# Kernel optimization log

Hardware: AMD Instinct MI355X
Metric: run time of the kernel (lower is better)

Reference implementation:

```python
import jax, jax.numpy as jnp
import numpy as np

N = 50000      # nodes
E = 1600000    # edges (before self loops)
B = 512        # graphs
D = 128        # gcn dim (constant across the 3 GAT layers)
H = 1024       # hidden_dim
O = 128        # output_dim
NEG_SLOPE = 0.2


def setup_inputs() -> dict:
    key = jax.random.key(0)
    ks = jax.random.split(key, 24)
    inp = {
        "x": jax.random.normal(ks[0], (N, D), jnp.float32),
        "edge_index": jax.random.randint(ks[1], (2, E), 0, N, dtype=jnp.int64),
        "edge_weight": jax.random.uniform(ks[2], (E,), jnp.float32),
        "batch": jnp.sort(jax.random.randint(ks[3], (N,), 0, B, dtype=jnp.int64)),
    }
    s = 1.0 / np.sqrt(D)
    for i in range(3):
        k = 4 + 4 * i
        inp[f"W{i+1}"] = jax.random.normal(ks[k], (D, D), jnp.float32) * s
        inp[f"as{i+1}"] = jax.random.normal(ks[k + 1], (D,), jnp.float32) * s
        inp[f"ad{i+1}"] = jax.random.normal(ks[k + 2], (D,), jnp.float32) * s
        inp[f"b{i+1}"] = jnp.zeros((D,), jnp.float32)
    inp["Wf1"] = jax.random.normal(ks[16], (D, H), jnp.float32) * s
    inp["bf1"] = jnp.zeros((H,), jnp.float32)
    inp["Wf2"] = jax.random.normal(ks[17], (H, O), jnp.float32) * (1.0 / np.sqrt(H))
    inp["bf2"] = jnp.zeros((O,), jnp.float32)
    return inp


def gat_conv(x, src, dst, W, a_src, a_dst, b):
    """PyG GATConv, heads=1: gather -> leakyrelu -> segment softmax -> scatter-add."""
    h = x @ W                                   # [N, D]
    e = jax.nn.leaky_relu(jnp.take(h @ a_src, src) + jnp.take(h @ a_dst, dst), NEG_SLOPE)  # [E']
    m = jax.ops.segment_max(e, dst, num_segments=N)
    ex = jnp.exp(e - m[dst])
    denom = jax.ops.segment_sum(ex, dst, num_segments=N)
    alpha = ex / denom[dst]                      # segment softmax over incoming edges
    out = jax.ops.segment_sum(alpha[:, None] * h[src], dst, num_segments=N)
    return out + b


def reference(x, edge_index, edge_weight, batch,
              W1, as1, ad1, b1, W2, as2, ad2, b2, W3, as3, ad3, b3,
              Wf1, bf1, Wf2, bf2):
    # GATConv adds self loops; edge_weight is unused by GATConv (faithful to original)
    loop = jnp.arange(N, dtype=edge_index.dtype)
    src = jnp.concatenate([edge_index[0], loop])
    dst = jnp.concatenate([edge_index[1], loop])

    h = gat_conv(x, src, dst, W1, as1, ad1, b1)
    h = jax.nn.relu(gat_conv(h, src, dst, W2, as2, ad2, b2))
    h = jax.nn.relu(gat_conv(h, src, dst, W3, as3, ad3, b3))

    # global mean pool (gep)
    sums = jax.ops.segment_sum(h, batch, num_segments=B)        # [B, D]
    counts = jax.ops.segment_sum(jnp.ones((N,), h.dtype), batch, num_segments=B)
    pooled = sums / jnp.maximum(counts, 1.0)[:, None]

    # MLP head; dropout is identity at inference
    o = jax.nn.relu(pooled) @ Wf1 + bf1
    o = jax.nn.relu(o) @ Wf2 + bf2
    return o
```

## Files before the change

kernel.cpp:

```cpp
#include <hip/hip_runtime.h>
#include <cstdint>
#include <cstddef>

#define NEG_SLOPE 0.2f

typedef _Float16 f16x8 __attribute__((ext_vector_type(8)));
typedef float f32x4v __attribute__((ext_vector_type(4)));

__device__ __forceinline__ unsigned enc_f(float f) {
  unsigned u = __float_as_uint(f);
  return (u & 0x80000000u) ? ~u : (u | 0x80000000u);
}
__device__ __forceinline__ float dec_f(unsigned u) {
  return (u & 0x80000000u) ? __uint_as_float(u ^ 0x80000000u) : __uint_as_float(~u);
}

#define AST 136
#define WST 136
#define HST 132
#define SMEM_BYTES (64 * AST * 2 + 128 * WST * 2)

__global__ void k_bounds(const int* __restrict__ batch, int N, int B,
                         int* __restrict__ gstart, unsigned* __restrict__ maxPart,
                         int* __restrict__ counts) {
  int n = blockIdx.x * blockDim.x + threadIdx.x;
  if (n < 768) maxPart[n] = 0u;
  if (n >= N) return;
  counts[n] = 0;
  int cur = batch[n];
  if (n == 0) {
    for (int g = 0; g <= cur; g++) gstart[g] = 0;
  } else {
    int prev = batch[n - 1];
    for (int g = prev + 1; g <= cur; g++) gstart[g] = n;
  }
  if (n == N - 1) {
    for (int g = cur + 1; g <= B; g++) gstart[g] = N;
  }
}

__global__ void k_count_rank(const int* __restrict__ dst, int E,
                             int* counts, int* __restrict__ rank) {
  int e = blockIdx.x * blockDim.x + threadIdx.x;
  if (e < E) rank[e] = atomicAdd(&counts[dst[e]], 1);
}

__global__ __launch_bounds__(1024) void k_scan1(const int* __restrict__ counts, int N,
                                                int* __restrict__ row_ptr, int* __restrict__ part) {
  __shared__ int tmp[1024];
  int t = threadIdx.x;
  int i = blockIdx.x * 1024 + t;
  int v = (i < N) ? 1 + counts[i] : 0;
  tmp[t] = v;
  __syncthreads();
  for (int off = 1; off < 1024; off <<= 1) {
    int u = (t >= off) ? tmp[t - off] : 0;
    __syncthreads();
    tmp[t] += u;
    __syncthreads();
  }
  if (i < N) row_ptr[i + 1] = tmp[t];
  if (t == 1023) part[blockIdx.x] = tmp[t];
}

__global__ __launch_bounds__(1024) void k_scan3(int* __restrict__ row_ptr,
                                                const int* __restrict__ part, int N) {
  __shared__ int s_off;
  int bi = blockIdx.x;
  if (threadIdx.x == 0) {
    int run = 0;
    for (int b = 0; b < bi; b++) run += part[b];
    s_off = run;
    if (bi == 0) row_ptr[0] = 0;
  }
  __syncthreads();
  int i = bi * 1024 + threadIdx.x;
  if (i < N) row_ptr[i + 1] += s_off;
}

__device__ __forceinline__ void gemm_body(char* smem, float* redmax, int bx,
                                          const float* __restrict__ A32,
                                          const unsigned short* __restrict__ A16,
                                          const float* __restrict__ W,
                                          unsigned short* __restrict__ hb,
                                          const float* __restrict__ asrc,
                                          const float* __restrict__ adst,
                                          float* __restrict__ sv, float* __restrict__ dv,
                                          unsigned* __restrict__ maxSlot, int M) {
  _Float16* Ah = (_Float16*)smem;
  _Float16* Wt = (_Float16*)(smem + 64 * AST * 2);
  float*    hS = (float*)(smem + 64 * AST * 2);
  int t = threadIdx.x;
  int rowbase = bx * 64;

  if (A16) {
    for (int i = t; i < 64 * 16; i += 256) {
      int r = i >> 4, c8 = (i & 15) << 3;
      int gr = rowbase + r;
      uint4 v = make_uint4(0u, 0u, 0u, 0u);
      if (gr < M) v = *(const uint4*)&A16[(size_t)gr * 128 + c8];
      *(uint4*)&Ah[r * AST + c8] = v;
    }
  } else {
    for (int i = t; i < 64 * 32; i += 256) {
      int r = i >> 5, c4 = (i & 31) << 2;
      int gr = rowbase + r;
      float4 v = make_float4(0.f, 0.f, 0.f, 0.f);
      if (gr < M) v = *(const float4*)&A32[(size_t)gr * 128 + c4];
      _Float16 tmp[4] = {(_Float16)v.x, (_Float16)v.y, (_Float16)v.z, (_Float16)v.w};
      *(short4*)&Ah[r * AST + c4] = *(short4*)tmp;
    }
  }
  for (int i = t; i < 128 * 32; i += 256) {
    int r = i >> 5, c4 = (i & 31) << 2;
    float4 v = *(const float4*)&W[(size_t)r * 128 + c4];
    Wt[(c4 + 0) * WST + r] = (_Float16)v.x;
    Wt[(c4 + 1) * WST + r] = (_Float16)v.y;
    Wt[(c4 + 2) * WST + r] = (_Float16)v.z;
    Wt[(c4 + 3) * WST + r] = (_Float16)v.w;
  }
  __syncthreads();

  int wave = t >> 6, lane = t & 63, quad = lane >> 4, l15 = lane & 15;
  f32x4v acc[4][2];
#pragma unroll
  for (int mt = 0; mt < 4; mt++)
#pragma unroll
    for (int nt = 0; nt < 2; nt++) {
      acc[mt][nt][0] = 0.f; acc[mt][nt][1] = 0.f; acc[mt][nt][2] = 0.f; acc[mt][nt][3] = 0.f;
    }

#pragma unroll
  for (int s = 0; s < 4; s++) {
    int k0 = (s << 5) + (quad << 3);
    f16x8 af[4], bf[2];
#pragma unroll
    for (int mt = 0; mt < 4; mt++)
      af[mt] = *(f16x8*)&Ah[(mt * 16 + l15) * AST + k0];
#pragma unroll
    for (int nt = 0; nt < 2; nt++)
      bf[nt] = *(f16x8*)&Wt[(wave * 32 + nt * 16 + l15) * WST + k0];
#pragma unroll
    for (int mt = 0; mt < 4; mt++)
#pragma unroll
      for (int nt = 0; nt < 2; nt++)
        acc[mt][nt] = __builtin_amdgcn_mfma_f32_16x16x32_f16(af[mt], bf[nt], acc[mt][nt], 0, 0, 0);
  }
  __syncthreads();

#pragma unroll
  for (int mt = 0; mt < 4; mt++)
#pragma unroll
    for (int nt = 0; nt < 2; nt++)
#pragma unroll
      for (int rr = 0; rr < 4; rr++)
        hS[(mt * 16 + quad * 4 + rr) * HST + wave * 32 + nt * 16 + l15] = acc[mt][nt][rr];
  __syncthreads();

  int tx = t & 31, ty = t >> 5;
  float4 av  = *(const float4*)&asrc[tx * 4];
  float4 adv = *(const float4*)&adst[tx * 4];
  float wmax = -1e30f;
#pragma unroll
  for (int r8 = 0; r8 < 8; r8++) {
    int row = r8 * 8 + ty;
    int gr = rowbase + row;
    float4 hv = *(float4*)&hS[row * HST + tx * 4];
    float ps = hv.x * av.x + hv.y * av.y + hv.z * av.z + hv.w * av.w;
    float pd = hv.x * adv.x + hv.y * adv.y + hv.z * adv.z + hv.w * adv.w;
#pragma unroll
    for (int mask = 16; mask; mask >>= 1) {
      ps += __shfl_xor(ps, mask);
      pd += __shfl_xor(pd, mask);
    }
    if (gr < M) {
      _Float16 hq[4] = {(_Float16)hv.x, (_Float16)hv.y, (_Float16)hv.z, (_Float16)hv.w};
      *(uint2*)&hb[(size_t)gr * 128 + tx * 4] = *(uint2*)hq;
      if (tx == 0) { sv[gr] = ps; dv[gr] = pd; wmax = fmaxf(wmax, ps); }
    }
  }
#pragma unroll
  for (int mask = 32; mask; mask >>= 1) wmax = fmaxf(wmax, __shfl_xor(wmax, mask));
  if ((t & 63) == 0) redmax[t >> 6] = wmax;
  __syncthreads();
  if (t == 0) {
    float mx = fmaxf(fmaxf(redmax[0], redmax[1]), fmaxf(redmax[2], redmax[3]));
    atomicMax(&maxSlot[bx & 255], enc_f(mx));
  }
}

__global__ __launch_bounds__(256) void k_fill_gemm(const int* __restrict__ src,
                                                   const int* __restrict__ dst,
                                                   const int* __restrict__ rank, int E, int N,
                                                   const int* __restrict__ row_ptr,
                                                   int* __restrict__ col,
                                                   const float* __restrict__ A32,
                                                   const float* __restrict__ W,
                                                   unsigned short* __restrict__ hb,
                                                   const float* __restrict__ asrc,
                                                   const float* __restrict__ adst,
                                                   float* __restrict__ sv, float* __restrict__ dv,
                                                   unsigned* __restrict__ maxSlot, int Gg) {
  __shared__ __align__(16) char smem[SMEM_BYTES];
  __shared__ float redmax[4];
  int b = (int)blockIdx.x;
  bool isGemm = ((b % 9) == 4) && ((b / 9) < Gg);
  if (isGemm) {
    gemm_body(smem, redmax, b / 9, A32, (const unsigned short*)nullptr, W,
              hb, asrc, adst, sv, dv, maxSlot, N);
  } else {
    int nGemmBefore = (b >= 4) ? min((b - 4) / 9 + 1, Gg) : 0;
    int i = (b - nGemmBefore) * 256 + threadIdx.x;
    if (i < N) col[row_ptr[i]] = i;
    int e = i - N;
    if (e >= 0 && e < E) col[row_ptr[dst[e]] + 1 + rank[e]] = src[e];
  }
}

__global__ __launch_bounds__(256) void k_gemm_fused(const unsigned short* __restrict__ A16,
                                                    const float* __restrict__ W,
                                                    unsigned short* __restrict__ hb,
                                                    const float* __restrict__ asrc,
                                                    const float* __restrict__ adst,
                                                    float* __restrict__ sv, float* __restrict__ dv,
                                                    unsigned* __restrict__ maxSlot, int M) {
  __shared__ __align__(16) char smem[SMEM_BYTES];
  __shared__ float redmax[4];
  gemm_body(smem, redmax, (int)blockIdx.x, (const float*)nullptr, A16, W,
            hb, asrc, adst, sv, dv, maxSlot, M);
}

__global__ __launch_bounds__(256) void k_agg(const unsigned short* __restrict__ hb,
                                             const float* __restrict__ sv,
                                             const float* __restrict__ dv,
                                             const int* __restrict__ row_ptr,
                                             const int* __restrict__ col,
                                             const float* __restrict__ bias,
                                             const unsigned* __restrict__ maxSlot,
                                             unsigned short* __restrict__ out16,
                                             int N, int relu) {
  int wid = (int)((blockIdx.x * (size_t)blockDim.x + threadIdx.x) >> 6);
  int lane = threadIdx.x & 63;
  if (wid >= N) return;

  unsigned mp = max(max(maxSlot[lane], maxSlot[lane + 64]),
                    max(maxSlot[lane + 128], maxSlot[lane + 192]));
#pragma unroll
  for (int off = 32; off; off >>= 1) mp = max(mp, __shfl_xor(mp, off));
  float maxS = dec_f(mp);

  int beg = row_ptr[wid], end = row_ptr[wid + 1];
  float dn = dv[wid];
  float m = maxS + dn;
  m = (m > 0.f) ? m : NEG_SLOPE * m;

  int g = lane >> 4, sub = lane & 15;
  const uint32_t* hbu = (const uint32_t*)hb;
  float acc[8];
#pragma unroll
  for (int k = 0; k < 8; k++) acc[k] = 0.f;
  float dsum = 0.f;

  int j = beg + g;
  float w0 = 0.f, w1 = 0.f, w2 = 0.f;
  uint4 h0 = make_uint4(0u, 0u, 0u, 0u);
  uint4 h1 = make_uint4(0u, 0u, 0u, 0u);
  uint4 h2 = make_uint4(0u, 0u, 0u, 0u);
  if (j < end) {
    int sn = col[j];
    float e = sv[sn] + dn;
    e = (e > 0.f) ? e : NEG_SLOPE * e;
    w0 = __expf(e - m);
    h0 = *(const uint4*)(hbu + (size_t)sn * 64 + sub * 4);
  }
  if (j + 4 < end) {
    int sn = col[j + 4];
    float e = sv[sn] + dn;
    e = (e > 0.f) ? e : NEG_SLOPE * e;
    w1 = __expf(e - m);
    h1 = *(const uint4*)(hbu + (size_t)sn * 64 + sub * 4);
  }
  if (j + 8 < end) {
    int sn = col[j + 8];
    float e = sv[sn] + dn;
    e = (e > 0.f) ? e : NEG_SLOPE * e;
    w2 = __expf(e - m);
    h2 = *(const uint4*)(hbu + (size_t)sn * 64 + sub * 4);
  }
  j += 12;
  while (j < end) {
    dsum += w0;
    {
      const _Float16* hp = (const _Float16*)&h0;
#pragma unroll
      for (int k = 0; k < 8; k++) acc[k] += w0 * (float)hp[k];
    }
    w0 = w1; h0 = h1;
    w1 = w2; h1 = h2;
    int sn = col[j];
    float e = sv[sn] + dn;
    e = (e > 0.f) ? e : NEG_SLOPE * e;
    w2 = __expf(e - m);
    h2 = *(const uint4*)(hbu + (size_t)sn * 64 + sub * 4);
    j += 4;
  }
  {
    dsum += w0;
    const _Float16* hp = (const _Float16*)&h0;
#pragma unroll
    for (int k = 0; k < 8; k++) acc[k] += w0 * (float)hp[k];
  }
  {
    dsum += w1;
    const _Float16* hp = (const _Float16*)&h1;
#pragma unroll
    for (int k = 0; k < 8; k++) acc[k] += w1 * (float)hp[k];
  }
  {
    dsum += w2;
    const _Float16* hp = (const _Float16*)&h2;
#pragma unroll
    for (int k = 0; k < 8; k++) acc[k] += w2 * (float)hp[k];
  }

  dsum += __shfl_xor(dsum, 16);
  dsum += __shfl_xor(dsum, 32);
#pragma unroll
  for (int k = 0; k < 8; k++) {
    acc[k] += __shfl_xor(acc[k], 16);
    acc[k] += __shfl_xor(acc[k], 32);
  }
  if (lane < 16) {
    float inv = 1.f / dsum;
    float o[8];
    const float* bp = &bias[sub * 8];
#pragma unroll
    for (int k = 0; k < 8; k++) {
      o[k] = acc[k] * inv + bp[k];
      if (relu) o[k] = fmaxf(o[k], 0.f);
    }
    _Float16 q[8];
#pragma unroll
    for (int k = 0; k < 8; k++) q[k] = (_Float16)o[k];
    *(uint4*)&out16[(size_t)wid * 128 + sub * 8] = *(uint4*)q;
  }
}

__global__ __launch_bounds__(256) void k_pool(const unsigned short* __restrict__ h16,
                                              const int* __restrict__ gstart,
                                              float* __restrict__ pooled, int B) {
  __shared__ float red[4][128];
  int b = blockIdx.x, t = threadIdx.x;
  int c = t & 63, seg = t >> 6;
  int s0 = gstart[b], s1 = gstart[b + 1];
  int cnt = s1 - s0;
  int per = (cnt + 3) >> 2;
  int n0 = s0 + seg * per;
  int n1 = min(n0 + per, s1);
  const uint32_t* hu = (const uint32_t*)h16;
  float a0 = 0.f, a1 = 0.f;
  for (int n = n0; n < n1; n++) {
    union { uint32_t u; _Float16 h[2]; } cv;
    cv.u = hu[(size_t)n * 64 + c];
    a0 += (float)cv.h[0];
    a1 += (float)cv.h[1];
  }
  if (seg) { red[seg][2 * c] = a0; red[seg][2 * c + 1] = a1; }
  __syncthreads();
  if (seg == 0) {
    a0 += red[1][2 * c] + red[2][2 * c] + red[3][2 * c];
    a1 += red[1][2 * c + 1] + red[2][2 * c + 1] + red[3][2 * c + 1];
    float inv = 1.f / (float)(cnt > 0 ? cnt : 1);
    pooled[b * 128 + 2 * c]     = fmaxf(a0 * inv, 0.f);
    pooled[b * 128 + 2 * c + 1] = fmaxf(a1 * inv, 0.f);
  }
}

__global__ __launch_bounds__(256) void k_mlp(const float* __restrict__ pooled,
                                             const float* __restrict__ Wf1,
                                             const float* __restrict__ bf1,
                                             const float* __restrict__ Wf2,
                                             const float* __restrict__ bf2,
                                             float* __restrict__ out, int B) {
  __shared__ float P[4][128];
  __shared__ float H1[4][1024];
  __shared__ float R[4][128];
  int t = threadIdx.x;
  int g0 = blockIdx.x * 4;

  for (int i = t; i < 4 * 128; i += 256) {
    int gi = i >> 7, c = i & 127;
    P[gi][c] = (g0 + gi < B) ? pooled[(size_t)(g0 + gi) * 128 + c] : 0.f;
  }
  __syncthreads();

#pragma unroll
  for (int cb = 0; cb < 4; cb++) {
    int c = cb * 256 + t;
    float a0 = 0.f, a1 = 0.f, a2 = 0.f, a3 = 0.f;
    for (int k = 0; k < 128; k++) {
      float w = Wf1[(size_t)k * 1024 + c];
      a0 += P[0][k] * w; a1 += P[1][k] * w; a2 += P[2][k] * w; a3 += P[3][k] * w;
    }
    float b = bf1[c];
    H1[0][c] = fmaxf(a0 + b, 0.f);
    H1[1][c] = fmaxf(a1 + b, 0.f);
    H1[2][c] = fmaxf(a2 + b, 0.f);
    H1[3][c] = fmaxf(a3 + b, 0.f);
  }
  __syncthreads();

  int c = t & 127, hh = t >> 7;
  float a0 = 0.f, a1 = 0.f, a2 = 0.f, a3 = 0.f;
  int k0 = hh * 512;
  for (int k = k0; k < k0 + 512; k++) {
    float w = Wf2[(size_t)k * 128 + c];
    a0 += H1[0][k] * w; a1 += H1[1][k] * w; a2 += H1[2][k] * w; a3 += H1[3][k] * w;
  }
  if (hh == 1) { R[0][c] = a0; R[1][c] = a1; R[2][c] = a2; R[3][c] = a3; }
  __syncthreads();
  if (hh == 0) {
    float b = bf2[c];
    float o0 = a0 + R[0][c] + b;
    float o1 = a1 + R[1][c] + b;
    float o2 = a2 + R[2][c] + b;
    float o3 = a3 + R[3][c] + b;
    if (g0 + 0 < B) out[(size_t)(g0 + 0) * 128 + c] = o0;
    if (g0 + 1 < B) out[(size_t)(g0 + 1) * 128 + c] = o1;
    if (g0 + 2 < B) out[(size_t)(g0 + 2) * 128 + c] = o2;
    if (g0 + 3 < B) out[(size_t)(g0 + 3) * 128 + c] = o3;
  }
}

extern "C" void kernel_launch(void* const* d_in, const int* in_sizes, int n_in,
                              void* d_out, int out_size, void* d_ws, size_t ws_size,
                              hipStream_t stream) {
  const float* x     = (const float*)d_in[0];
  const int*   ei    = (const int*)d_in[1];
  const int*   batch = (const int*)d_in[3];
  const float* W1 = (const float*)d_in[4];
  const float* as1 = (const float*)d_in[5];
  const float* ad1 = (const float*)d_in[6];
  const float* b1 = (const float*)d_in[7];
  const float* W2 = (const float*)d_in[8];
  const float* as2 = (const float*)d_in[9];
  const float* ad2 = (const float*)d_in[10];
  const float* b2 = (const float*)d_in[11];
  const float* W3 = (const float*)d_in[12];
  const float* as3 = (const float*)d_in[13];
  const float* ad3 = (const float*)d_in[14];
  const float* b3 = (const float*)d_in[15];
  const float* Wf1 = (const float*)d_in[16];
  const float* bf1 = (const float*)d_in[17];
  const float* Wf2 = (const float*)d_in[18];
  const float* bf2 = (const float*)d_in[19];

  const int N = in_sizes[0] / 128;
  const int E = in_sizes[1] / 2;
  const int B = out_size / 128;

  char* base_ws = (char*)d_ws;
  size_t off = 0;
  auto carve = [&](size_t bytes) -> void* {
    off = (off + 255) & ~(size_t)255;
    void* p = base_ws + off;
    off += bytes;
    return p;
  };
  int* counts   = (int*)carve((size_t)N * 4);
  int* row_ptr  = (int*)carve((size_t)(N + 1) * 4);
  int* rank     = (int*)carve((size_t)E * 4);
  int* col      = (int*)carve((size_t)(E + N) * 4);
  int* part     = (int*)carve(1024 * 4);
  int* gstart   = (int*)carve((size_t)(B + 1) * 4);
  unsigned* maxPart = (unsigned*)carve(768 * 4);
  float* sbuf   = (float*)carve((size_t)N * 4);
  float* dbuf   = (float*)carve((size_t)N * 4);
  unsigned short* hb  = (unsigned short*)carve((size_t)N * 128 * 2);
  unsigned short* a16 = (unsigned short*)carve((size_t)N * 128 * 2);
  float* pooled = (float*)carve((size_t)B * 128 * 4);

  const int* srcp = ei;
  const int* dstp = ei + E;
  const int nb = (N + 1023) / 1024;
  const int Gg = (N + 63) / 64;
  const int Gf = (E + N + 255) / 256;

  hipLaunchKernelGGL(k_bounds, dim3((N + 255) / 256), dim3(256), 0, stream,
                     batch, N, B, gstart, maxPart, counts);
  hipLaunchKernelGGL(k_count_rank, dim3((E + 255) / 256), dim3(256), 0, stream,
                     dstp, E, counts, rank);
  hipLaunchKernelGGL(k_scan1, dim3(nb), dim3(1024), 0, stream, counts, N, row_ptr, part);
  hipLaunchKernelGGL(k_scan3, dim3(nb), dim3(1024), 0, stream, row_ptr, part, N);

  hipLaunchKernelGGL(k_fill_gemm, dim3(Gf + Gg), dim3(256), 0, stream,
                     srcp, dstp, rank, E, N, row_ptr, col,
                     x, W1, hb, as1, ad1, sbuf, dbuf, maxPart + 0 * 256, Gg);

  hipLaunchKernelGGL(k_agg, dim3((N + 3) / 4), dim3(256), 0, stream,
                     hb, sbuf, dbuf, row_ptr, col, b1, maxPart + 0 * 256, a16, N, 0);

  hipLaunchKernelGGL(k_gemm_fused, dim3(Gg), dim3(256), 0, stream,
                     a16, W2, hb, as2, ad2, sbuf, dbuf, maxPart + 1 * 256, N);
  hipLaunchKernelGGL(k_agg, dim3((N + 3) / 4), dim3(256), 0, stream,
                     hb, sbuf, dbuf, row_ptr, col, b2, maxPart + 1 * 256, a16, N, 1);

  hipLaunchKernelGGL(k_gemm_fused, dim3(Gg), dim3(256), 0, stream,
                     a16, W3, hb, as3, ad3, sbuf, dbuf, maxPart + 2 * 256, N);
  hipLaunchKernelGGL(k_agg, dim3((N + 3) / 4), dim3(256), 0, stream,
                     hb, sbuf, dbuf, row_ptr, col, b3, maxPart + 2 * 256, a16, N, 1);

  hipLaunchKernelGGL(k_pool, dim3(B), dim3(256), 0, stream, a16, gstart, pooled, B);
  hipLaunchKernelGGL(k_mlp, dim3((B + 3) / 4), dim3(256), 0, stream,
                     pooled, Wf1, bf1, Wf2, bf2, (float*)d_out, B);
}
```

Baseline: 543.0 us.

## Fuse layer-1 GEMM with edge counting; batch neighbor indices per wave in aggregation

```diff
diff --git a/kernel.cpp b/kernel.cpp
--- a/kernel.cpp
+++ b/kernel.cpp
@@ -37,12 +37,6 @@
   if (n == N - 1) {
     for (int g = cur + 1; g <= B; g++) gstart[g] = N;
   }
-}
-
-__global__ void k_count_rank(const int* __restrict__ dst, int E,
-                             int* counts, int* __restrict__ rank) {
-  int e = blockIdx.x * blockDim.x + threadIdx.x;
-  if (e < E) rank[e] = atomicAdd(&counts[dst[e]], 1);
 }
 
 __global__ __launch_bounds__(1024) void k_scan1(const int* __restrict__ counts, int N,
@@ -189,32 +183,38 @@
   }
 }
 
-__global__ __launch_bounds__(256) void k_fill_gemm(const int* __restrict__ src,
-                                                   const int* __restrict__ dst,
-                                                   const int* __restrict__ rank, int E, int N,
-                                                   const int* __restrict__ row_ptr,
-                                                   int* __restrict__ col,
-                                                   const float* __restrict__ A32,
-                                                   const float* __restrict__ W,
-                                                   unsigned short* __restrict__ hb,
-                                                   const float* __restrict__ asrc,
-                                                   const float* __restrict__ adst,
-                                                   float* __restrict__ sv, float* __restrict__ dv,
-                                                   unsigned* __restrict__ maxSlot, int Gg) {
+__global__ __launch_bounds__(256) void k_count_gemm(const int* __restrict__ dst, int E,
+                                                    int* counts, int* __restrict__ rank,
+                                                    const float* __restrict__ A32,
+                                                    const float* __restrict__ W,
+                                                    unsigned short* __restrict__ hb,
+                                                    const float* __restrict__ asrc,
+                                                    const float* __restrict__ adst,
+                                                    float* __restrict__ sv, float* __restrict__ dv,
+                                                    unsigned* __restrict__ maxSlot, int Gg, int N) {
   __shared__ __align__(16) char smem[SMEM_BYTES];
   __shared__ float redmax[4];
   int b = (int)blockIdx.x;
-  bool isGemm = ((b % 9) == 4) && ((b / 9) < Gg);
+  bool isGemm = ((b & 7) == 4) && ((b >> 3) < Gg);
   if (isGemm) {
-    gemm_body(smem, redmax, b / 9, A32, (const unsigned short*)nullptr, W,
+    gemm_body(smem, redmax, b >> 3, A32, (const unsigned short*)nullptr, W,
               hb, asrc, adst, sv, dv, maxSlot, N);
   } else {
-    int nGemmBefore = (b >= 4) ? min((b - 4) / 9 + 1, Gg) : 0;
-    int i = (b - nGemmBefore) * 256 + threadIdx.x;
-    if (i < N) col[row_ptr[i]] = i;
-    int e = i - N;
-    if (e >= 0 && e < E) col[row_ptr[dst[e]] + 1 + rank[e]] = src[e];
-  }
+    int nGemmBefore = (b >= 4) ? min((b - 4) / 8 + 1, Gg) : 0;
+    int e = (b - nGemmBefore) * 256 + threadIdx.x;
+    if (e < E) rank[e] = atomicAdd(&counts[dst[e]], 1);
+  }
+}
+
+__global__ __launch_bounds__(256) void k_fill(const int* __restrict__ src,
+                                              const int* __restrict__ dst,
+                                              const int* __restrict__ rank, int E, int N,
+                                              const int* __restrict__ row_ptr,
+                                              int* __restrict__ col) {
+  int i = blockIdx.x * 256 + threadIdx.x;
+  if (i < N) col[row_ptr[i]] = i;
+  int e = i - N;
+  if (e >= 0 && e < E) col[row_ptr[dst[e]] + 1 + rank[e]] = src[e];
 }
 
 __global__ __launch_bounds__(256) void k_gemm_fused(const unsigned short* __restrict__ A16,
@@ -261,70 +261,45 @@
   for (int k = 0; k < 8; k++) acc[k] = 0.f;
   float dsum = 0.f;
 
-  int j = beg + g;
-  float w0 = 0.f, w1 = 0.f, w2 = 0.f;
-  uint4 h0 = make_uint4(0u, 0u, 0u, 0u);
-  uint4 h1 = make_uint4(0u, 0u, 0u, 0u);
-  uint4 h2 = make_uint4(0u, 0u, 0u, 0u);
-  if (j < end) {
-    int sn = col[j];
-    float e = sv[sn] + dn;
-    e = (e > 0.f) ? e : NEG_SLOPE * e;
-    w0 = __expf(e - m);
-    h0 = *(const uint4*)(hbu + (size_t)sn * 64 + sub * 4);
-  }
-  if (j + 4 < end) {
-    int sn = col[j + 4];
-    float e = sv[sn] + dn;
-    e = (e > 0.f) ? e : NEG_SLOPE * e;
-    w1 = __expf(e - m);
-    h1 = *(const uint4*)(hbu + (size_t)sn * 64 + sub * 4);
-  }
-  if (j + 8 < end) {
-    int sn = col[j + 8];
-    float e = sv[sn] + dn;
-    e = (e > 0.f) ? e : NEG_SLOPE * e;
-    w2 = __expf(e - m);
-    h2 = *(const uint4*)(hbu + (size_t)sn * 64 + sub * 4);
-  }
-  j += 12;
-  while (j < end) {
-    dsum += w0;
+  for (int base = beg; base < end; base += 64) {
+    int cnt = min(end - base, 64);
+
+    int sn_l = 0;
+    float w_l = 0.f;
+    if (lane < cnt) {
+      sn_l = col[base + lane];
+      float e = sv[sn_l] + dn;
+      e = (e > 0.f) ? e : NEG_SLOPE * e;
+      w_l = __expf(e - m);
+      dsum += w_l;
+    }
+
+    int kmaxW = (cnt + 3) >> 2;
+    int sl0 = g;
+    int sn0 = __shfl(sn_l, sl0);
+    float w0 = __shfl(w_l, sl0);
+    uint4 h0 = make_uint4(0u, 0u, 0u, 0u);
+    if (sl0 < cnt) h0 = *(const uint4*)(hbu + (size_t)sn0 * 64 + sub * 4);
+    for (int k = 1; k < kmaxW; k++) {
+      int sl = (k << 2) + g;
+      int sn1 = __shfl(sn_l, sl);
+      float w1 = __shfl(w_l, sl);
+      uint4 h1 = make_uint4(0u, 0u, 0u, 0u);
+      if (sl < cnt) h1 = *(const uint4*)(hbu + (size_t)sn1 * 64 + sub * 4);
+      const _Float16* hp = (const _Float16*)&h0;
+#pragma unroll
+      for (int q = 0; q < 8; q++) acc[q] += w0 * (float)hp[q];
+      w0 = w1; h0 = h1;
+    }
     {
       const _Float16* hp = (const _Float16*)&h0;
 #pragma unroll
-      for (int k = 0; k < 8; k++) acc[k] += w0 * (float)hp[k];
-    }
-    w0 = w1; h0 = h1;
-    w1 = w2; h1 = h2;
-    int sn = col[j];
-    float e = sv[sn] + dn;
-    e = (e > 0.f) ? e : NEG_SLOPE * e;
-    w2 = __expf(e - m);
-    h2 = *(const uint4*)(hbu + (size_t)sn * 64 + sub * 4);
-    j += 4;
-  }
-  {
-    dsum += w0;
-    const _Float16* hp = (const _Float16*)&h0;
-#pragma unroll
-    for (int k = 0; k < 8; k++) acc[k] += w0 * (float)hp[k];
-  }
-  {
-    dsum += w1;
-    const _Float16* hp = (const _Float16*)&h1;
-#pragma unroll
-    for (int k = 0; k < 8; k++) acc[k] += w1 * (float)hp[k];
-  }
-  {
-    dsum += w2;
-    const _Float16* hp = (const _Float16*)&h2;
-#pragma unroll
-    for (int k = 0; k < 8; k++) acc[k] += w2 * (float)hp[k];
-  }
-
-  dsum += __shfl_xor(dsum, 16);
-  dsum += __shfl_xor(dsum, 32);
+      for (int q = 0; q < 8; q++) acc[q] += w0 * (float)hp[q];
+    }
+  }
+
+#pragma unroll
+  for (int off = 1; off < 64; off <<= 1) dsum += __shfl_xor(dsum, off);
 #pragma unroll
   for (int k = 0; k < 8; k++) {
     acc[k] += __shfl_xor(acc[k], 16);
@@ -484,18 +459,21 @@
   const int* dstp = ei + E;
   const int nb = (N + 1023) / 1024;
   const int Gg = (N + 63) / 64;
+  const int Cb = (E + 255) / 256;
   const int Gf = (E + N + 255) / 256;
 
   hipLaunchKernelGGL(k_bounds, dim3((N + 255) / 256), dim3(256), 0, stream,
                      batch, N, B, gstart, maxPart, counts);
-  hipLaunchKernelGGL(k_count_rank, dim3((E + 255) / 256), dim3(256), 0, stream,
-                     dstp, E, counts, rank);
+
+  hipLaunchKernelGGL(k_count_gemm, dim3(Cb + Gg), dim3(256), 0, stream,
+                     dstp, E, counts, rank,
+                     x, W1, hb, as1, ad1, sbuf, dbuf, maxPart + 0 * 256, Gg, N);
+
   hipLaunchKernelGGL(k_scan1, dim3(nb), dim3(1024), 0, stream, counts, N, row_ptr, part);
   hipLaunchKernelGGL(k_scan3, dim3(nb), dim3(1024), 0, stream, row_ptr, part, N);
 
-  hipLaunchKernelGGL(k_fill_gemm, dim3(Gf + Gg), dim3(256), 0, stream,
-                     srcp, dstp, rank, E, N, row_ptr, col,
-                     x, W1, hb, as1, ad1, sbuf, dbuf, maxPart + 0 * 256, Gg);
+  hipLaunchKernelGGL(k_fill, dim3(Gf), dim3(256), 0, stream,
+                     srcp, dstp, rank, E, N, row_ptr, col);
 
   hipLaunchKernelGGL(k_agg, dim3((N + 3) / 4), dim3(256), 0, stream,
                      hb, sbuf, dbuf, row_ptr, col, b1, maxPart + 0 * 256, a16, N, 0);
```

Result: slower. 605.4 us (+11.5%).
